# Kernel optimization log

Measured on AMD Instinct MI355X. Metric: run time of the kernel, lower is better.

The kernel has to match this reference:

```python
import jax, jax.numpy as jnp
import numpy as np


def _segsum(x):
    """Stable segment sum: exp(segsum(A)) is 1-semiseparable. x: (..., T) -> (..., T, T)."""
    T = x.shape[-1]
    xx = jnp.broadcast_to(x[..., None], (*x.shape, T))
    xx = jnp.where(jnp.tril(jnp.ones((T, T), bool), -1), xx, 0.0)
    s = jnp.cumsum(xx, axis=-2)
    return jnp.where(jnp.tril(jnp.ones((T, T), bool), 0), s, -jnp.inf)


def setup_inputs() -> dict:
    key = jax.random.key(0)
    ks = jax.random.split(key, 6)
    b, T, h, p, n = 2, 1024, 32, 64, 128
    x = jax.random.normal(ks[0], (b, T, h, p), jnp.float32)
    # negative decay rates, as produced by -exp(A_log)*softplus(dt) in Mamba2
    A = -jax.random.uniform(ks[1], (b, T, h), jnp.float32, minval=0.01, maxval=0.5)
    B = jax.random.normal(ks[2], (b, T, h, n), jnp.float32)
    C = jax.random.normal(ks[3], (b, T, h, n), jnp.float32)
    # retrieval similarity mask (lower-triangular, like segment_and_cosine_similarity output)
    L_mask = jax.random.uniform(ks[4], (b, h, T, T), jnp.float32) * jnp.tril(jnp.ones((T, T), jnp.float32))
    mask_scaling_factor = jnp.float32(0.5)
    return {"x": x, "A": A, "B": B, "C": C, "L_mask": L_mask,
            "mask_scaling_factor": mask_scaling_factor, "chunk_size": 64}


def reference(x, A, B, C, L_mask, mask_scaling_factor, chunk_size):
    b, T, h, p = x.shape
    n = B.shape[-1]
    l = chunk_size
    k = T // l
    # chunk: b (c l) ... -> b c l ...
    xr = x.reshape(b, k, l, h, p)
    Br = B.reshape(b, k, l, h, n)
    Cr = C.reshape(b, k, l, h, n)
    Ar = jnp.transpose(A.reshape(b, k, l, h), (0, 3, 1, 2))  # b h c l
    A_cs = jnp.cumsum(Ar, axis=-1)                            # b h c l
    L = jnp.exp(_segsum(Ar))                                  # b h c l l
    # decompose_diagonal_and_lower_tri(L_mask, chunk_size)
    r = L_mask.reshape(b, h, k, l, k, l)
    didx = np.arange(k)
    L_mask_diag = jnp.moveaxis(r[:, :, didx, :, didx, :], 0, 2)          # b h k l l
    row_idx, col_idx = np.tril_indices(k, -1)                             # strict lower block pairs
    lower_tri = jnp.moveaxis(r[:, :, row_idx, :, col_idx, :], 0, 2)       # b h P l l
    L = L + mask_scaling_factor * L_mask_diag
    # diagonal (intra-chunk) blocks
    Y_diag = jnp.einsum('bclhn,bcshn,bhcls,bcshp->bclhp', Cr, Br, L, xr)
    # retrieval off-diagonal blocks, scatter-added back per destination chunk
    Y_tmp = jnp.einsum('bclhn,bcshn,bhcls,bcshp->bclhp',
                       Cr[:, row_idx], Br[:, col_idx],
                       mask_scaling_factor * lower_tri, xr[:, col_idx])   # b P l h p
    Y_retr = jnp.moveaxis(
        jax.ops.segment_sum(jnp.moveaxis(Y_tmp, 1, 0), jnp.asarray(row_idx), num_segments=k),
        0, 1)                                                             # b k l h p
    # inter-chunk state passing
    decay_states = jnp.exp(A_cs[..., -1:] - A_cs)                         # b h c l
    states = jnp.einsum('bclhn,bhcl,bclhp->bchpn', Br, decay_states, xr)  # b c h p n
    states = jnp.concatenate([jnp.zeros_like(states[:, :1]), states], axis=1)
    decay_chunk = jnp.exp(_segsum(jnp.pad(A_cs[..., -1], ((0, 0), (0, 0), (1, 0)))))  # b h (k+1) (k+1)
    new_states = jnp.einsum('bhzc,bchpn->bzhpn', decay_chunk, states)
    states_in, final_state = new_states[:, :-1], new_states[:, -1]
    Y_off = jnp.einsum('bclhn,bchpn,bhcl->bclhp', Cr, states_in, jnp.exp(A_cs))
    Y = (Y_diag + Y_off + Y_retr).reshape(b, T, h, p)
    return Y, final_state
```

## Files before the change

### kernel.cpp

```cpp
#include <hip/hip_runtime.h>

#define T_ 1024
#define H_ 32
#define P_ 64
#define N_ 128
#define L_ 64

typedef float f32x4 __attribute__((ext_vector_type(4)));
typedef short short8 __attribute__((ext_vector_type(8)));
typedef short short4v __attribute__((ext_vector_type(4)));
typedef unsigned int uint2v __attribute__((ext_vector_type(2)));
typedef unsigned int uint4v __attribute__((ext_vector_type(4)));

#define LOG2E 1.4426950408889634f

static __device__ __forceinline__ float bf2f(short s) {
  return __uint_as_float(((unsigned int)(unsigned short)s) << 16);
}

static __device__ __forceinline__ unsigned cvt_pk_bf16(float lo, float hi) {
  unsigned r;
  asm("v_cvt_pk_bf16_f32 %0, %1, %2" : "=v"(r) : "v"(lo), "v"(hi));
  return r;
}

static __device__ __forceinline__ float fexp2(float x) {
#if __has_builtin(__builtin_amdgcn_exp2f)
  return __builtin_amdgcn_exp2f(x);
#else
  return __expf(x * 0.6931471805599453f);
#endif
}

__global__ __launch_bounds__(1024) void cuma_kernel(const float* __restrict__ A,
                                                    float* __restrict__ cumA) {
  const int bh = blockIdx.x;
  const int b = bh >> 5, h = bh & 31;
  const int t = threadIdx.x;
  __shared__ float s[1024];
  s[t] = A[(b * T_ + t) * H_ + h];
  __syncthreads();
  for (int off = 1; off < 1024; off <<= 1) {
    float v = (t >= off) ? s[t - off] : 0.0f;
    __syncthreads();
    s[t] += v;
    __syncthreads();
  }
  cumA[bh * T_ + t] = s[t] * LOG2E;
}

__global__ __launch_bounds__(256) void prep_kernel(
    const float* __restrict__ x, const float* __restrict__ Bm,
    const float* __restrict__ Cm, short* __restrict__ Bbf,
    short* __restrict__ BT, short* __restrict__ Cbf,
    short* __restrict__ xT) {
  const int bh = blockIdx.x;
  const int tb = blockIdx.y;
  const int b = bh >> 5, h = bh & 31;
  const int tid = threadIdx.x;
  __shared__ short Bt[128][72];
  __shared__ short Xt[64][72];

#pragma unroll
  for (int i = 0; i < 8; ++i) {
    const int idx = tid + 256 * i;
    const int row = idx >> 5, n4 = idx & 31;
    const float4 v = *(const float4*)(Bm + ((size_t)(b * T_ + tb * 64 + row) * H_ + h) * N_ + n4 * 4);
    const unsigned p0 = cvt_pk_bf16(v.x, v.y);
    const unsigned p1 = cvt_pk_bf16(v.z, v.w);
    uint2v o; o.x = p0; o.y = p1;
    *(uint2v*)(Bbf + ((size_t)bh * T_ + tb * 64 + row) * N_ + n4 * 4) = o;
    Bt[n4 * 4 + 0][row] = (short)p0; Bt[n4 * 4 + 1][row] = (short)(p0 >> 16);
    Bt[n4 * 4 + 2][row] = (short)p1; Bt[n4 * 4 + 3][row] = (short)(p1 >> 16);
  }
#pragma unroll
  for (int i = 0; i < 8; ++i) {
    const int idx = tid + 256 * i;
    const int row = idx >> 5, n4 = idx & 31;
    const float4 v = *(const float4*)(Cm + ((size_t)(b * T_ + tb * 64 + row) * H_ + h) * N_ + n4 * 4);
    uint2v o; o.x = cvt_pk_bf16(v.x, v.y); o.y = cvt_pk_bf16(v.z, v.w);
    *(uint2v*)(Cbf + ((size_t)bh * T_ + tb * 64 + row) * N_ + n4 * 4) = o;
  }
#pragma unroll
  for (int i = 0; i < 4; ++i) {
    const int idx = tid + 256 * i;
    const int row = idx >> 4, p4 = idx & 15;
    const float4 v = *(const float4*)(x + ((size_t)(b * T_ + tb * 64 + row) * H_ + h) * P_ + p4 * 4);
    const unsigned p0 = cvt_pk_bf16(v.x, v.y);
    const unsigned p1 = cvt_pk_bf16(v.z, v.w);
    Xt[p4 * 4 + 0][row] = (short)p0;
    Xt[p4 * 4 + 1][row] = (short)(p0 >> 16);
    Xt[p4 * 4 + 2][row] = (short)p1;
    Xt[p4 * 4 + 3][row] = (short)(p1 >> 16);
  }
  __syncthreads();
#pragma unroll
  for (int i = 0; i < 4; ++i) {
    const int idx = tid + 256 * i;
    const int n = idx >> 3, t8 = idx & 7;
    const short4v a = *(const short4v*)&Bt[n][t8 * 8];
    const short4v c = *(const short4v*)&Bt[n][t8 * 8 + 4];
    short8 o;
    o[0] = a.x; o[1] = a.y; o[2] = a.z; o[3] = a.w;
    o[4] = c.x; o[5] = c.y; o[6] = c.z; o[7] = c.w;
    *(short8*)(BT + ((size_t)bh * N_ + n) * T_ + tb * 64 + t8 * 8) = o;
  }
#pragma unroll
  for (int i = 0; i < 2; ++i) {
    const int idx = tid + 256 * i;
    const int p = idx >> 3, t8 = idx & 7;
    const short4v a = *(const short4v*)&Xt[p][t8 * 8];
    const short4v c = *(const short4v*)&Xt[p][t8 * 8 + 4];
    short8 o;
    o[0] = a.x; o[1] = a.y; o[2] = a.z; o[3] = a.w;
    o[4] = c.x; o[5] = c.y; o[6] = c.z; o[7] = c.w;
    *(short8*)(xT + ((size_t)bh * P_ + p) * T_ + tb * 64 + t8 * 8) = o;
  }
}

__global__ __launch_bounds__(256, 2) void attn_kernel(
    const short* __restrict__ xT, const short* __restrict__ Bbf,
    const short* __restrict__ Cbf, const float* __restrict__ mask,
    const float* __restrict__ msf_p, const float* __restrict__ cumA,
    float* __restrict__ Y) {
  const int blk = blockIdx.x;
  const int bh = blk & 63;
  const int jj = blk >> 6;
  const int b = bh >> 5, h = bh & 31;
  const float msf = msf_p[0];
  const int tid = threadIdx.x;
  const int w = tid >> 6;
  const int lane = tid & 63;
  const int q = lane >> 4, c = lane & 15;

  __shared__ short Ps[4][16][72];

  const short* Bg0 = Bbf + (size_t)bh * T_ * N_ + 8 * q;
  const short* xg0 = xT + (size_t)bh * P_ * T_ + 8 * q;

#pragma unroll 1
  for (int pass = 0; pass < 2; ++pass) {
    const int qc = pass ? jj : (15 - jj);

    short8 cf[4];
    {
      const short* Cg = Cbf + ((size_t)bh * T_ + qc * L_ + 16 * w + c) * N_ + 8 * q;
#pragma unroll
      for (int kt = 0; kt < 4; ++kt) cf[kt] = *(const short8*)(Cg + kt * 32);
    }
    float ca_i[4];
#pragma unroll
    for (int r = 0; r < 4; ++r)
      ca_i[r] = cumA[bh * T_ + qc * L_ + 16 * w + 4 * q + r];

    f32x4 yacc[4];
#pragma unroll
    for (int pt = 0; pt < 4; ++pt) yacc[pt] = (f32x4){0.f, 0.f, 0.f, 0.f};

    const float* mrow0 = mask + ((size_t)bh * T_ + (size_t)(qc * L_ + 16 * w + 4 * q)) * T_ + c;

    float mvA[16], mvB[16], ckA[4], ckB[4];
#pragma unroll
    for (int tj = 0; tj < 4; ++tj)
#pragma unroll
      for (int r = 0; r < 4; ++r)
        mvA[tj * 4 + r] = __builtin_nontemporal_load(mrow0 + (size_t)r * T_ + 16 * tj);
#pragma unroll
    for (int tj = 0; tj < 4; ++tj) ckA[tj] = cumA[bh * T_ + 16 * tj + c];

#define ATTN_STEP(KC, MVI, CKI, MVO, CKO)                                      \
  {                                                                            \
    const int kc_ = (KC);                                                      \
    const int kcn_ = (kc_ + 1 <= qc) ? (kc_ + 1) : qc;                         \
    short8 bfr[16];                                                            \
    const short* Bg = Bg0 + (size_t)kc_ * L_ * N_;                             \
    _Pragma("unroll") for (int kt = 0; kt < 4; ++kt)                           \
        _Pragma("unroll") for (int tj = 0; tj < 4; ++tj)                       \
            bfr[kt * 4 + tj] =                                                 \
        *(const short8*)(Bg + (size_t)(16 * tj + c) * N_ + kt * 32);           \
    short8 xfr[8];                                                             \
    const short* xg = xg0 + kc_ * L_;                                          \
    _Pragma("unroll") for (int kt2 = 0; kt2 < 2; ++kt2)                        \
        _Pragma("unroll") for (int pt = 0; pt < 4; ++pt)                       \
            xfr[kt2 * 4 + pt] =                                                \
        *(const short8*)(xg + (size_t)(16 * pt + c) * T_ + kt2 * 32);          \
    const float* mb = mrow0 + (size_t)kcn_ * L_;                               \
    _Pragma("unroll") for (int tj = 0; tj < 4; ++tj)                           \
        _Pragma("unroll") for (int r = 0; r < 4; ++r)                          \
            MVO[tj * 4 + r] =                                                  \
        __builtin_nontemporal_load(mb + (size_t)r * T_ + 16 * tj);             \
    _Pragma("unroll") for (int tj = 0; tj < 4; ++tj)                           \
        CKO[tj] = cumA[bh * T_ + kcn_ * L_ + 16 * tj + c];                     \
    f32x4 sacc[4];                                                             \
    _Pragma("unroll") for (int tj = 0; tj < 4; ++tj)                           \
        sacc[tj] = (f32x4){0.f, 0.f, 0.f, 0.f};                                \
    _Pragma("unroll") for (int kt = 0; kt < 4; ++kt)                           \
        _Pragma("unroll") for (int tj = 0; tj < 4; ++tj)                       \
            sacc[tj] = __builtin_amdgcn_mfma_f32_16x16x32_bf16(                \
        cf[kt], bfr[kt * 4 + tj], sacc[tj], 0, 0, 0);                          \
    const bool diag = (kc_ == qc);                                             \
    _Pragma("unroll") for (int tj = 0; tj < 4; ++tj) {                         \
      const int j_l = 16 * tj + c;                                             \
      float fv[4];                                                             \
      _Pragma("unroll") for (int r = 0; r < 4; ++r) {                          \
        const int i_l = 16 * w + 4 * q + r;                                    \
        float wgt = fexp2(ca_i[r] - CKI[tj]) + msf * MVI[tj * 4 + r];          \
        if (diag && j_l > i_l) wgt = 0.0f;                                     \
        fv[r] = sacc[tj][r] * wgt;                                             \
      }                                                                        \
      const unsigned p0 = cvt_pk_bf16(fv[0], fv[1]);                           \
      const unsigned p1 = cvt_pk_bf16(fv[2], fv[3]);                           \
      Ps[w][4 * q + 0][j_l] = (short)p0;                                       \
      Ps[w][4 * q + 1][j_l] = (short)(p0 >> 16);                               \
      Ps[w][4 * q + 2][j_l] = (short)p1;                                       \
      Ps[w][4 * q + 3][j_l] = (short)(p1 >> 16);                               \
    }                                                                          \
    _Pragma("unroll") for (int kt2 = 0; kt2 < 2; ++kt2) {                      \
      const short8 pf = *(const short8*)&Ps[w][c][kt2 * 32 + 8 * q];           \
      _Pragma("unroll") for (int pt = 0; pt < 4; ++pt)                         \
          yacc[pt] = __builtin_amdgcn_mfma_f32_16x16x32_bf16(                  \
          pf, xfr[kt2 * 4 + pt], yacc[pt], 0, 0, 0);                           \
    }                                                                          \
  }

    int kc = 0;
    for (; kc + 1 <= qc; kc += 2) {
      ATTN_STEP(kc, mvA, ckA, mvB, ckB)
      ATTN_STEP(kc + 1, mvB, ckB, mvA, ckA)
    }
    if (kc <= qc) {
      ATTN_STEP(kc, mvA, ckA, mvB, ckB)
    }
#undef ATTN_STEP

    float* Yg = Y + ((size_t)(b * T_ + qc * L_ + 16 * w + 4 * q) * H_ + h) * P_;
#pragma unroll
    for (int pt = 0; pt < 4; ++pt)
#pragma unroll
      for (int r = 0; r < 4; ++r)
        __builtin_nontemporal_store(yacc[pt][r], Yg + (size_t)r * (H_ * P_) + 16 * pt + c);
  }
}

__global__ __launch_bounds__(256) void zero_fs(float* __restrict__ fs) {
  const int i = blockIdx.x * 256 + threadIdx.x;
  ((float4*)fs)[i] = make_float4(0.f, 0.f, 0.f, 0.f);
}

__global__ __launch_bounds__(256) void state_kernel(
    const short* __restrict__ xT, const short* __restrict__ BT,
    const float* __restrict__ cumA, float* __restrict__ out) {
  const int bh = blockIdx.x;
  const int tq = blockIdx.y;
  const int tid = threadIdx.x;
  const int w = tid >> 6;
  const int lane = tid & 63;
  const int q = lane >> 4, c = lane & 15;

  __shared__ float wsh[256];
  {
    const float cend = cumA[bh * T_ + (T_ - 1)];
    wsh[tid] = fexp2(cend - cumA[bh * T_ + tq * 256 + tid]);
  }
  __syncthreads();

  f32x4 acc[8];
#pragma unroll
  for (int nt = 0; nt < 8; ++nt) acc[nt] = (f32x4){0.f, 0.f, 0.f, 0.f};

#pragma unroll
  for (int ktl = 0; ktl < 8; ++ktl) {
    const int t0 = ktl * 32;
    const int tg = tq * 256 + t0;
    const short8 xv = *(const short8*)(xT + ((size_t)bh * P_ + 16 * w + c) * T_ + tg + 8 * q);
    const float4 w0 = *(const float4*)&wsh[t0 + 8 * q];
    const float4 w1 = *(const float4*)&wsh[t0 + 8 * q + 4];
    const float a0 = bf2f(xv[0]) * w0.x, a1 = bf2f(xv[1]) * w0.y;
    const float a2 = bf2f(xv[2]) * w0.z, a3 = bf2f(xv[3]) * w0.w;
    const float a4 = bf2f(xv[4]) * w1.x, a5 = bf2f(xv[5]) * w1.y;
    const float a6 = bf2f(xv[6]) * w1.z, a7 = bf2f(xv[7]) * w1.w;
    uint4v uu;
    uu.x = cvt_pk_bf16(a0, a1); uu.y = cvt_pk_bf16(a2, a3);
    uu.z = cvt_pk_bf16(a4, a5); uu.w = cvt_pk_bf16(a6, a7);
    const short8 af = __builtin_bit_cast(short8, uu);
#pragma unroll
    for (int nt = 0; nt < 8; ++nt) {
      const short8 bf = *(const short8*)(BT + ((size_t)bh * N_ + 16 * nt + c) * T_ + tg + 8 * q);
      acc[nt] = __builtin_amdgcn_mfma_f32_16x16x32_bf16(af, bf, acc[nt], 0, 0, 0);
    }
  }

  float* o = out + (size_t)bh * P_ * N_;
#pragma unroll
  for (int nt = 0; nt < 8; ++nt)
#pragma unroll
    for (int r = 0; r < 4; ++r)
      atomicAdd(&o[(size_t)(16 * w + 4 * q + r) * N_ + 16 * nt + c], acc[nt][r]);
}

extern "C" void kernel_launch(void* const* d_in, const int* in_sizes, int n_in,
                              void* d_out, int out_size, void* d_ws, size_t ws_size,
                              hipStream_t stream) {
  const float* x    = (const float*)d_in[0];
  const float* A    = (const float*)d_in[1];
  const float* Bm   = (const float*)d_in[2];
  const float* Cm   = (const float*)d_in[3];
  const float* mask = (const float*)d_in[4];
  const float* msf  = (const float*)d_in[5];
  float* Y  = (float*)d_out;
  float* fs = (float*)d_out + (size_t)2 * T_ * H_ * P_;

  char* ws = (char*)d_ws;
  float* cumA = (float*)ws;
  size_t off = 1 << 18;
  short* Bbf = (short*)(ws + off); off += (size_t)64 * T_ * N_ * 2;
  short* BT  = (short*)(ws + off); off += (size_t)64 * T_ * N_ * 2;
  short* Cbf = (short*)(ws + off); off += (size_t)64 * T_ * N_ * 2;
  short* xT  = (short*)(ws + off);

  cuma_kernel<<<64, 1024, 0, stream>>>(A, cumA);
  prep_kernel<<<dim3(64, 16), 256, 0, stream>>>(x, Bm, Cm, Bbf, BT, Cbf, xT);
  attn_kernel<<<512, 256, 0, stream>>>(xT, Bbf, Cbf, mask, msf, cumA, Y);
  zero_fs<<<512, 256, 0, stream>>>(fs);
  state_kernel<<<dim3(64, 4), 256, 0, stream>>>(xT, BT, cumA, fs);
}
```

Before: 499.8 us.

## Fuse cumsum into prep, software-pipeline attention loop, split state kernel over N

The separate cumsum kernel is folded into the prep kernel as an extra block row, which removes one launch. The attention loop is restructured so the P@x MFMA for the previous chunk overlaps the score MFMA for the current chunk. Decay weights are precomputed one step ahead and s_setprio is added around the MFMA blocks. The state kernel now splits work over the N dimension instead of time, so it writes results directly, which removes the zero-fill kernel and the atomics. In exchange the attention step holds more registers and the prep kernel carries an extra branch.

```diff
diff --git a/kernel.cpp b/kernel.cpp
--- a/kernel.cpp
+++ b/kernel.cpp
@@ -32,32 +32,43 @@
 #endif
 }
 
-__global__ __launch_bounds__(1024) void cuma_kernel(const float* __restrict__ A,
-                                                    float* __restrict__ cumA) {
-  const int bh = blockIdx.x;
-  const int b = bh >> 5, h = bh & 31;
-  const int t = threadIdx.x;
-  __shared__ float s[1024];
-  s[t] = A[(b * T_ + t) * H_ + h];
-  __syncthreads();
-  for (int off = 1; off < 1024; off <<= 1) {
-    float v = (t >= off) ? s[t - off] : 0.0f;
-    __syncthreads();
-    s[t] += v;
-    __syncthreads();
-  }
-  cumA[bh * T_ + t] = s[t] * LOG2E;
-}
-
 __global__ __launch_bounds__(256) void prep_kernel(
     const float* __restrict__ x, const float* __restrict__ Bm,
-    const float* __restrict__ Cm, short* __restrict__ Bbf,
-    short* __restrict__ BT, short* __restrict__ Cbf,
-    short* __restrict__ xT) {
+    const float* __restrict__ Cm, const float* __restrict__ A,
+    short* __restrict__ Bbf, short* __restrict__ BT,
+    short* __restrict__ Cbf, short* __restrict__ xT,
+    float* __restrict__ cumA) {
   const int bh = blockIdx.x;
   const int tb = blockIdx.y;
   const int b = bh >> 5, h = bh & 31;
   const int tid = threadIdx.x;
+
+  if (tb == 16) {
+    __shared__ float sc[256];
+    const int t0 = 4 * tid;
+    const float a0 = A[(size_t)(b * T_ + t0 + 0) * H_ + h];
+    const float a1 = A[(size_t)(b * T_ + t0 + 1) * H_ + h];
+    const float a2 = A[(size_t)(b * T_ + t0 + 2) * H_ + h];
+    const float a3 = A[(size_t)(b * T_ + t0 + 3) * H_ + h];
+    const float p1 = a0 + a1, p2 = p1 + a2, p3 = p2 + a3;
+    sc[tid] = p3;
+    __syncthreads();
+    for (int off = 1; off < 256; off <<= 1) {
+      float v = (tid >= off) ? sc[tid - off] : 0.0f;
+      __syncthreads();
+      sc[tid] += v;
+      __syncthreads();
+    }
+    const float base = sc[tid] - p3;
+    float4 o;
+    o.x = (base + a0) * LOG2E;
+    o.y = (base + p1) * LOG2E;
+    o.z = (base + p2) * LOG2E;
+    o.w = (base + p3) * LOG2E;
+    *(float4*)(cumA + (size_t)bh * T_ + t0) = o;
+    return;
+  }
+
   __shared__ short Bt[128][72];
   __shared__ short Xt[64][72];
 
@@ -159,16 +170,24 @@
 
     const float* mrow0 = mask + ((size_t)bh * T_ + (size_t)(qc * L_ + 16 * w + 4 * q)) * T_ + c;
 
-    float mvA[16], mvB[16], ckA[4], ckB[4];
-#pragma unroll
-    for (int tj = 0; tj < 4; ++tj)
-#pragma unroll
-      for (int r = 0; r < 4; ++r)
-        mvA[tj * 4 + r] = __builtin_nontemporal_load(mrow0 + (size_t)r * T_ + 16 * tj);
-#pragma unroll
-    for (int tj = 0; tj < 4; ++tj) ckA[tj] = cumA[bh * T_ + 16 * tj + c];
-
-#define ATTN_STEP(KC, MVI, CKI, MVO, CKO)                                      \
+    float wgA[16], wgB[16];
+    {
+      float mv[16], ck[4];
+#pragma unroll
+      for (int tj = 0; tj < 4; ++tj)
+#pragma unroll
+        for (int r = 0; r < 4; ++r)
+          mv[tj * 4 + r] = __builtin_nontemporal_load(mrow0 + (size_t)r * T_ + 16 * tj);
+#pragma unroll
+      for (int tj = 0; tj < 4; ++tj) ck[tj] = cumA[bh * T_ + 16 * tj + c];
+#pragma unroll
+      for (int tj = 0; tj < 4; ++tj)
+#pragma unroll
+        for (int r = 0; r < 4; ++r)
+          wgA[tj * 4 + r] = fexp2(ca_i[r] - ck[tj]) + msf * mv[tj * 4 + r];
+    }
+
+#define ATTN_STEP(KC, WGI, WGO, DOPV)                                          \
   {                                                                            \
     const int kc_ = (KC);                                                      \
     const int kcn_ = (kc_ + 1 <= qc) ? (kc_ + 1) : qc;                         \
@@ -179,59 +198,95 @@
             bfr[kt * 4 + tj] =                                                 \
         *(const short8*)(Bg + (size_t)(16 * tj + c) * N_ + kt * 32);           \
     short8 xfr[8];                                                             \
-    const short* xg = xg0 + kc_ * L_;                                          \
-    _Pragma("unroll") for (int kt2 = 0; kt2 < 2; ++kt2)                        \
-        _Pragma("unroll") for (int pt = 0; pt < 4; ++pt)                       \
-            xfr[kt2 * 4 + pt] =                                                \
-        *(const short8*)(xg + (size_t)(16 * pt + c) * T_ + kt2 * 32);          \
+    if (DOPV) {                                                                \
+      const short* xg = xg0 + (kc_ - 1) * L_;                                  \
+      _Pragma("unroll") for (int kt2 = 0; kt2 < 2; ++kt2)                      \
+          _Pragma("unroll") for (int pt = 0; pt < 4; ++pt)                     \
+              xfr[kt2 * 4 + pt] =                                              \
+          *(const short8*)(xg + (size_t)(16 * pt + c) * T_ + kt2 * 32);        \
+    }                                                                          \
+    float mv_[16], ck_[4];                                                     \
     const float* mb = mrow0 + (size_t)kcn_ * L_;                               \
     _Pragma("unroll") for (int tj = 0; tj < 4; ++tj)                           \
         _Pragma("unroll") for (int r = 0; r < 4; ++r)                          \
-            MVO[tj * 4 + r] =                                                  \
+            mv_[tj * 4 + r] =                                                  \
         __builtin_nontemporal_load(mb + (size_t)r * T_ + 16 * tj);             \
     _Pragma("unroll") for (int tj = 0; tj < 4; ++tj)                           \
-        CKO[tj] = cumA[bh * T_ + kcn_ * L_ + 16 * tj + c];                     \
+        ck_[tj] = cumA[bh * T_ + kcn_ * L_ + 16 * tj + c];                     \
     f32x4 sacc[4];                                                             \
     _Pragma("unroll") for (int tj = 0; tj < 4; ++tj)                           \
         sacc[tj] = (f32x4){0.f, 0.f, 0.f, 0.f};                                \
+    __builtin_amdgcn_s_setprio(1);                                             \
     _Pragma("unroll") for (int kt = 0; kt < 4; ++kt)                           \
         _Pragma("unroll") for (int tj = 0; tj < 4; ++tj)                       \
             sacc[tj] = __builtin_amdgcn_mfma_f32_16x16x32_bf16(                \
         cf[kt], bfr[kt * 4 + tj], sacc[tj], 0, 0, 0);                          \
+    __builtin_amdgcn_s_setprio(0);                                             \
+    _Pragma("unroll") for (int tj = 0; tj < 4; ++tj)                           \
+        _Pragma("unroll") for (int r = 0; r < 4; ++r)                          \
+            WGO[tj * 4 + r] =                                                  \
+        fexp2(ca_i[r] - ck_[tj]) + msf * mv_[tj * 4 + r];                      \
     const bool diag = (kc_ == qc);                                             \
+    unsigned pw[8];                                                            \
     _Pragma("unroll") for (int tj = 0; tj < 4; ++tj) {                         \
       const int j_l = 16 * tj + c;                                             \
       float fv[4];                                                             \
       _Pragma("unroll") for (int r = 0; r < 4; ++r) {                          \
         const int i_l = 16 * w + 4 * q + r;                                    \
-        float wgt = fexp2(ca_i[r] - CKI[tj]) + msf * MVI[tj * 4 + r];          \
-        if (diag && j_l > i_l) wgt = 0.0f;                                     \
-        fv[r] = sacc[tj][r] * wgt;                                             \
+        fv[r] = (diag && j_l > i_l) ? 0.f : sacc[tj][r] * WGI[tj * 4 + r];     \
       }                                                                        \
-      const unsigned p0 = cvt_pk_bf16(fv[0], fv[1]);                           \
-      const unsigned p1 = cvt_pk_bf16(fv[2], fv[3]);                           \
-      Ps[w][4 * q + 0][j_l] = (short)p0;                                       \
-      Ps[w][4 * q + 1][j_l] = (short)(p0 >> 16);                               \
-      Ps[w][4 * q + 2][j_l] = (short)p1;                                       \
-      Ps[w][4 * q + 3][j_l] = (short)(p1 >> 16);                               \
+      pw[tj * 2 + 0] = cvt_pk_bf16(fv[0], fv[1]);                              \
+      pw[tj * 2 + 1] = cvt_pk_bf16(fv[2], fv[3]);                              \
     }                                                                          \
-    _Pragma("unroll") for (int kt2 = 0; kt2 < 2; ++kt2) {                      \
-      const short8 pf = *(const short8*)&Ps[w][c][kt2 * 32 + 8 * q];           \
-      _Pragma("unroll") for (int pt = 0; pt < 4; ++pt)                         \
-          yacc[pt] = __builtin_amdgcn_mfma_f32_16x16x32_bf16(                  \
-          pf, xfr[kt2 * 4 + pt], yacc[pt], 0, 0, 0);                           \
+    if (DOPV) {                                                                \
+      __builtin_amdgcn_s_setprio(1);                                           \
+      _Pragma("unroll") for (int kt2 = 0; kt2 < 2; ++kt2) {                    \
+        const short8 pf = *(const short8*)&Ps[w][c][kt2 * 32 + 8 * q];         \
+        _Pragma("unroll") for (int pt = 0; pt < 4; ++pt)                       \
+            yacc[pt] = __builtin_amdgcn_mfma_f32_16x16x32_bf16(                \
+            pf, xfr[kt2 * 4 + pt], yacc[pt], 0, 0, 0);                         \
+      }                                                                        \
+      __builtin_amdgcn_s_setprio(0);                                           \
     }                                                                          \
-  }
-
-    int kc = 0;
+    _Pragma("unroll") for (int tj = 0; tj < 4; ++tj) {                         \
+      const int j_l = 16 * tj + c;                                             \
+      Ps[w][4 * q + 0][j_l] = (short)pw[tj * 2 + 0];                           \
+      Ps[w][4 * q + 1][j_l] = (short)(pw[tj * 2 + 0] >> 16);                   \
+      Ps[w][4 * q + 2][j_l] = (short)pw[tj * 2 + 1];                           \
+      Ps[w][4 * q + 3][j_l] = (short)(pw[tj * 2 + 1] >> 16);                   \
+    }                                                                          \
+  }
+
+    ATTN_STEP(0, wgA, wgB, 0)
+    int kc = 1;
     for (; kc + 1 <= qc; kc += 2) {
-      ATTN_STEP(kc, mvA, ckA, mvB, ckB)
-      ATTN_STEP(kc + 1, mvB, ckB, mvA, ckA)
+      ATTN_STEP(kc, wgB, wgA, 1)
+      ATTN_STEP(kc + 1, wgA, wgB, 1)
     }
     if (kc <= qc) {
-      ATTN_STEP(kc, mvA, ckA, mvB, ckB)
+      ATTN_STEP(kc, wgB, wgA, 1)
     }
 #undef ATTN_STEP
+
+    {
+      short8 xfr[8];
+      const short* xg = xg0 + qc * L_;
+#pragma unroll
+      for (int kt2 = 0; kt2 < 2; ++kt2)
+#pragma unroll
+        for (int pt = 0; pt < 4; ++pt)
+          xfr[kt2 * 4 + pt] = *(const short8*)(xg + (size_t)(16 * pt + c) * T_ + kt2 * 32);
+      __builtin_amdgcn_s_setprio(1);
+#pragma unroll
+      for (int kt2 = 0; kt2 < 2; ++kt2) {
+        const short8 pf = *(const short8*)&Ps[w][c][kt2 * 32 + 8 * q];
+#pragma unroll
+        for (int pt = 0; pt < 4; ++pt)
+          yacc[pt] = __builtin_amdgcn_mfma_f32_16x16x32_bf16(
+              pf, xfr[kt2 * 4 + pt], yacc[pt], 0, 0, 0);
+      }
+      __builtin_amdgcn_s_setprio(0);
+    }
 
     float* Yg = Y + ((size_t)(b * T_ + qc * L_ + 16 * w + 4 * q) * H_ + h) * P_;
 #pragma unroll
@@ -240,41 +295,39 @@
       for (int r = 0; r < 4; ++r)
         __builtin_nontemporal_store(yacc[pt][r], Yg + (size_t)r * (H_ * P_) + 16 * pt + c);
   }
-}
-
-__global__ __launch_bounds__(256) void zero_fs(float* __restrict__ fs) {
-  const int i = blockIdx.x * 256 + threadIdx.x;
-  ((float4*)fs)[i] = make_float4(0.f, 0.f, 0.f, 0.f);
 }
 
 __global__ __launch_bounds__(256) void state_kernel(
     const short* __restrict__ xT, const short* __restrict__ BT,
     const float* __restrict__ cumA, float* __restrict__ out) {
   const int bh = blockIdx.x;
-  const int tq = blockIdx.y;
+  const int nh = blockIdx.y;
   const int tid = threadIdx.x;
   const int w = tid >> 6;
   const int lane = tid & 63;
   const int q = lane >> 4, c = lane & 15;
 
-  __shared__ float wsh[256];
+  __shared__ float wsh[1024];
   {
     const float cend = cumA[bh * T_ + (T_ - 1)];
-    wsh[tid] = fexp2(cend - cumA[bh * T_ + tq * 256 + tid]);
+    const float4 cv = *(const float4*)(cumA + (size_t)bh * T_ + 4 * tid);
+    wsh[4 * tid + 0] = fexp2(cend - cv.x);
+    wsh[4 * tid + 1] = fexp2(cend - cv.y);
+    wsh[4 * tid + 2] = fexp2(cend - cv.z);
+    wsh[4 * tid + 3] = fexp2(cend - cv.w);
   }
   __syncthreads();
 
-  f32x4 acc[8];
-#pragma unroll
-  for (int nt = 0; nt < 8; ++nt) acc[nt] = (f32x4){0.f, 0.f, 0.f, 0.f};
-
-#pragma unroll
-  for (int ktl = 0; ktl < 8; ++ktl) {
-    const int t0 = ktl * 32;
-    const int tg = tq * 256 + t0;
+  f32x4 acc[2];
+#pragma unroll
+  for (int nt = 0; nt < 2; ++nt) acc[nt] = (f32x4){0.f, 0.f, 0.f, 0.f};
+
+#pragma unroll 4
+  for (int ktl = 0; ktl < 32; ++ktl) {
+    const int tg = ktl * 32;
     const short8 xv = *(const short8*)(xT + ((size_t)bh * P_ + 16 * w + c) * T_ + tg + 8 * q);
-    const float4 w0 = *(const float4*)&wsh[t0 + 8 * q];
-    const float4 w1 = *(const float4*)&wsh[t0 + 8 * q + 4];
+    const float4 w0 = *(const float4*)&wsh[tg + 8 * q];
+    const float4 w1 = *(const float4*)&wsh[tg + 8 * q + 4];
     const float a0 = bf2f(xv[0]) * w0.x, a1 = bf2f(xv[1]) * w0.y;
     const float a2 = bf2f(xv[2]) * w0.z, a3 = bf2f(xv[3]) * w0.w;
     const float a4 = bf2f(xv[4]) * w1.x, a5 = bf2f(xv[5]) * w1.y;
@@ -284,18 +337,19 @@
     uu.z = cvt_pk_bf16(a4, a5); uu.w = cvt_pk_bf16(a6, a7);
     const short8 af = __builtin_bit_cast(short8, uu);
 #pragma unroll
-    for (int nt = 0; nt < 8; ++nt) {
-      const short8 bf = *(const short8*)(BT + ((size_t)bh * N_ + 16 * nt + c) * T_ + tg + 8 * q);
+    for (int nt = 0; nt < 2; ++nt) {
+      const short8 bf = *(const short8*)(BT + ((size_t)bh * N_ + 32 * nh + 16 * nt + c) * T_ + tg + 8 * q);
       acc[nt] = __builtin_amdgcn_mfma_f32_16x16x32_bf16(af, bf, acc[nt], 0, 0, 0);
     }
   }
 
   float* o = out + (size_t)bh * P_ * N_;
 #pragma unroll
-  for (int nt = 0; nt < 8; ++nt)
+  for (int nt = 0; nt < 2; ++nt)
 #pragma unroll
     for (int r = 0; r < 4; ++r)
-      atomicAdd(&o[(size_t)(16 * w + 4 * q + r) * N_ + 16 * nt + c], acc[nt][r]);
+      __builtin_nontemporal_store(
+          acc[nt][r], o + (size_t)(16 * w + 4 * q + r) * N_ + 32 * nh + 16 * nt + c);
 }
 
 extern "C" void kernel_launch(void* const* d_in, const int* in_sizes, int n_in,
@@ -318,9 +372,7 @@
   short* Cbf = (short*)(ws + off); off += (size_t)64 * T_ * N_ * 2;
   short* xT  = (short*)(ws + off);
 
-  cuma_kernel<<<64, 1024, 0, stream>>>(A, cumA);
-  prep_kernel<<<dim3(64, 16), 256, 0, stream>>>(x, Bm, Cm, Bbf, BT, Cbf, xT);
+  prep_kernel<<<dim3(64, 17), 256, 0, stream>>>(x, Bm, Cm, A, Bbf, BT, Cbf, xT, cumA);
   attn_kernel<<<512, 256, 0, stream>>>(xT, Bbf, Cbf, mask, msf, cumA, Y);
-  zero_fs<<<512, 256, 0, stream>>>(fs);
   state_kernel<<<dim3(64, 4), 256, 0, stream>>>(xT, BT, cumA, fs);
 }
```

After: 491.5 us. Within noise of the previous version (-1.7%).
